# Kernel optimization log

Hardware: AMD Instinct MI355X
Metric: run time of the kernel (lower is better)

Reference implementation:

```python
import jax, jax.numpy as jnp
import numpy as np

N = 50000
E = 800000
F_IN, F_HID, F_OUT = 128, 128, 64


def setup_inputs() -> dict:
    key = jax.random.key(0)
    ks = jax.random.split(key, 8)
    x = jax.random.normal(ks[0], (N, F_IN), dtype=jnp.float32)
    attn_edge_index = jax.random.randint(ks[1], (2, E), 0, N, dtype=jnp.int64)
    attn_edge_weight = jax.random.uniform(ks[2], (E,), dtype=jnp.float32)
    # GCNConv params (glorot-ish scale); PyG lin has no bias, conv bias added after aggregation
    W1 = jax.random.normal(ks[3], (F_IN, F_HID), dtype=jnp.float32) * (1.0 / np.sqrt(F_IN))
    b1 = jnp.zeros((F_HID,), dtype=jnp.float32)
    W2 = jax.random.normal(ks[4], (F_HID, F_OUT), dtype=jnp.float32) * (1.0 / np.sqrt(F_HID))
    b2 = jnp.zeros((F_OUT,), dtype=jnp.float32)
    return {"x": x, "attn_edge_index": attn_edge_index, "attn_edge_weight": attn_edge_weight,
            "W1": W1, "b1": b1, "W2": W2, "b2": b2}


def _gcn_norm(edge_index, edge_weight, num_nodes):
    # Add self-loops with weight 1 (PyG gcn_norm default)
    loop = jnp.arange(num_nodes, dtype=edge_index.dtype)
    src = jnp.concatenate([edge_index[0], loop])
    dst = jnp.concatenate([edge_index[1], loop])
    w = jnp.concatenate([edge_weight, jnp.ones((num_nodes,), edge_weight.dtype)])
    deg = jax.ops.segment_sum(w, dst, num_segments=num_nodes)  # in-degree weighted
    dinv = jnp.where(deg > 0, jax.lax.rsqrt(deg), 0.0)
    norm = dinv[src] * w * dinv[dst]  # symmetric normalization
    return src, dst, norm


def _gcn_conv(h, src, dst, norm, W, b, num_nodes):
    h = h @ W                                   # [N, Fout] dense transform
    msg = norm[:, None] * h[src]                # [E+N, Fout] gather-multiply
    out = jax.ops.segment_sum(msg, dst, num_segments=num_nodes)  # scatter-add
    return out + b


def reference(x, attn_edge_index, attn_edge_weight, W1, b1, W2, b2):
    num_nodes = x.shape[0]
    src, dst, norm = _gcn_norm(attn_edge_index, attn_edge_weight, num_nodes)
    h = _gcn_conv(x, src, dst, norm, W1, b1, num_nodes)
    h = jax.nn.relu(h)
    # dropout(p=0.5) is identity in eval mode
    h = _gcn_conv(h, src, dst, norm, W2, b2, num_nodes)
    return h
```

## Files before the change

### kernel.cpp

```cpp
#include <hip/hip_runtime.h>
#include <hip/hip_bf16.h>

static constexpr int FIN   = 128;
static constexpr int FHID  = 128;
static constexpr int FOUTC = 64;
static constexpr int CAP   = 64;

typedef short bf16x8 __attribute__((ext_vector_type(8)));
typedef float f32x4 __attribute__((ext_vector_type(4)));
typedef unsigned u32x2 __attribute__((ext_vector_type(2)));
typedef unsigned u32x4 __attribute__((ext_vector_type(4)));

__device__ __forceinline__ float bfbits2f(unsigned short u) {
  union { unsigned i; float f; } c; c.i = ((unsigned)u) << 16; return c.f;
}
__device__ __forceinline__ float wbits2f(unsigned u) {
  union { unsigned i; float f; } c; c.i = u; return c.f;
}
__device__ __forceinline__ unsigned f2wbits(float f) {
  union { float fv; unsigned i; } c; c.fv = f; return c.i;
}
__device__ __forceinline__ void unpack_bf2(unsigned u, float& lo, float& hi) {
  union { unsigned i; float f; } a, b;
  a.i = u << 16;
  b.i = u & 0xffff0000u;
  lo = a.f; hi = b.f;
}
__device__ __forceinline__ unsigned short f2bfbits(float f) {
  union { float fv; unsigned i; } c; c.fv = f;
  unsigned i = c.i;
  unsigned r = i + 0x7FFFu + ((i >> 16) & 1u);
  if ((i & 0x7F800000u) == 0x7F800000u) r = i;
  return (unsigned short)(r >> 16);
}
__device__ __forceinline__ int ld_idx(const void* ei, int is64, long long off) {
  return is64 ? (int)((const long long*)ei)[off] : ((const int*)ei)[off];
}
__device__ __forceinline__ float ld_f(const void* p, int isbf, long long i) {
  return isbf ? bfbits2f(((const unsigned short*)p)[i]) : ((const float*)p)[i];
}

__global__ void setup_kernel(const unsigned short* __restrict__ xb,
                             const unsigned* __restrict__ eiw,
                             const void* __restrict__ W1, const void* __restrict__ W2,
                             int* __restrict__ flags, unsigned short* __restrict__ Wt1,
                             unsigned short* __restrict__ Wt2, uint4* __restrict__ ellz,
                             int nell4) {
  const int tid = threadIdx.x;
  const int gid = blockIdx.x * 256 + tid;
  __shared__ int sflags[2];
  if (tid < 64) {
    unsigned short xs = xb[2 * tid];
    unsigned long long mb = __ballot(((xs >> 7) & 0xFFu) >= 0xC0u);
    unsigned long long m2 = __ballot(eiw[2 * tid + 1] != 0u);
    if (tid == 0) {
      sflags[0] = (mb == 0ull);
      sflags[1] = (m2 == 0ull);
      if (blockIdx.x == 0) { flags[0] = sflags[0]; flags[1] = sflags[1]; }
    }
  }
  __syncthreads();
  int f = sflags[0];
  if (blockIdx.x < 96) {
    int i = gid;
    if (i < 128 * 128) {
      int k = i >> 7, nn = i & 127;
      Wt1[nn * 128 + k] = f2bfbits(ld_f(W1, f, i));
    } else {
      int j = i - 128 * 128;
      int k = j >> 6, nn = j & 63;
      Wt2[nn * 128 + k] = f2bfbits(ld_f(W2, f, j));
    }
  }
  uint4 z = make_uint4(0u, 0u, 0u, 0u);
  for (int j = gid; j < nell4; j += gridDim.x * 256) ellz[j] = z;
}

__global__ void fill_ell(const void* __restrict__ ei, const void* __restrict__ ew,
                         const int* __restrict__ flg, unsigned long long* __restrict__ ell,
                         int E, int half) {
  int g = blockIdx.x * 256 + threadIdx.x;
  if (g >= half) return;
  int is64 = flg[1], isbf = flg[0];
  int sA = ld_idx(ei, is64, g);
  int dA = ld_idx(ei, is64, (long long)E + g);
  unsigned wA = f2wbits(ld_f(ew, isbf, g));
  int eB = g + half;
  bool hasB = eB < E;
  int sB = 0, dB = 0;
  unsigned wB = 0u;
  if (hasB) {
    sB = ld_idx(ei, is64, eB);
    dB = ld_idx(ei, is64, (long long)E + eB);
    wB = f2wbits(ld_f(ew, isbf, eB));
  }
  unsigned long long vA = ((unsigned long long)wA << 32) | (unsigned)sA;
  unsigned long long vB = ((unsigned long long)wB << 32) | (unsigned)sB;
  unsigned long long* rowA = ell + (size_t)dA * CAP;
  unsigned long long* rowB = ell + (size_t)dB * CAP;
  int pA = g & (CAP - 1), pB = eB & (CAP - 1);
  bool doneA = (vA == 0ull);
  bool doneB = !hasB || (vB == 0ull);
  unsigned long long oA = doneA ? 0ull : atomicCAS(&rowA[pA], 0ull, vA);
  unsigned long long oB = doneB ? 0ull : atomicCAS(&rowB[pB], 0ull, vB);
  for (int t = 1; t < CAP && !doneA && oA != 0ull; ++t) {
    pA = (pA + 1) & (CAP - 1);
    oA = atomicCAS(&rowA[pA], 0ull, vA);
  }
  for (int t = 1; t < CAP && !doneB && oB != 0ull; ++t) {
    pB = (pB + 1) & (CAP - 1);
    oB = atomicCAS(&rowB[pB], 0ull, vB);
  }
}

__global__ void dinv_compact(uint2* __restrict__ ell, float* __restrict__ dinv,
                             unsigned* __restrict__ cedge, int n) {
  int wid = (blockIdx.x * 256 + threadIdx.x) >> 6;
  int lane = threadIdx.x & 63;
  if (wid >= n) return;
  u32x2 rv = __builtin_nontemporal_load((const u32x2*)(ell + (size_t)wid * CAP) + lane);
  float w = wbits2f(rv.y);
  float ws = w;
#pragma unroll
  for (int off = 1; off < 64; off <<= 1) ws += __shfl_xor(ws, off);
  bool valid = rv.y != 0u;
  unsigned long long m = __ballot(valid);
  int c = __popcll(m);
  int rank = __popcll(m & ((1ull << lane) - 1ull));
  int destl = valid ? rank : c + (lane - rank);
  unsigned entry = valid ? ((rv.x << 16) | (unsigned)f2bfbits(w)) : 0u;
  int pe = __builtin_amdgcn_ds_permute(destl << 2, (int)entry);
  cedge[(size_t)wid * (CAP * 2) + lane] = (unsigned)pe;
  if (lane == 0) dinv[wid] = rsqrtf(1.f + ws);
}

__launch_bounds__(256)
__global__ void gather_l1(const void* __restrict__ x, const int* __restrict__ flg,
                          const unsigned* __restrict__ cedge, const float* __restrict__ dinv,
                          unsigned* __restrict__ agg, int n) {
  int wid = (blockIdx.x * 256 + threadIdx.x) >> 6;
  int lane = threadIdx.x & 63;
  if (wid >= n) return;
  unsigned e = __builtin_nontemporal_load(cedge + (size_t)wid * (CAP * 2) + lane);
  unsigned long long m = __ballot(e != 0u);
  int c = __popcll(m);
  float di = dinv[wid];
  int rs = (lane < c) ? (int)(e >> 16) : wid;
  float dsrc = dinv[rs];
  float wv = (lane < c) ? bfbits2f((unsigned short)(e & 0xFFFFu)) : 1.f;
  int cp = c + 1; if (cp > 64) cp = 64;
  float rw = (lane < cp) ? wv * dsrc : 0.f;
  int iters = (cp + 15) >> 4;

  if (flg[0]) {
    const uint4* xv = (const uint4*)x;
    const int fgrp = lane & 15, egrp = lane >> 4;
    float acc[8];
#pragma unroll
    for (int k = 0; k < 8; ++k) acc[k] = 0.f;

#define L1_LOAD(UA, UB, UC, UD, WA, WB, WC, WD, base)                       \
    {                                                                       \
      int i0 = (base) + egrp, i1 = i0 + 4, i2 = i0 + 8, i3 = i0 + 12;       \
      int s0 = __shfl(rs, i0), s1 = __shfl(rs, i1);                         \
      int s2 = __shfl(rs, i2), s3 = __shfl(rs, i3);                         \
      UA = xv[(size_t)s0 * 16 + fgrp];                                      \
      UB = xv[(size_t)s1 * 16 + fgrp];                                      \
      UC = xv[(size_t)s2 * 16 + fgrp];                                      \
      UD = xv[(size_t)s3 * 16 + fgrp];                                      \
      WA = __shfl(rw, i0); WB = __shfl(rw, i1);                             \
      WC = __shfl(rw, i2); WD = __shfl(rw, i3);                             \
    }
#define L1_FMA(U, W)                                                        \
    { float l, h;                                                           \
      unpack_bf2(U.x, l, h); acc[0]=fmaf(W,l,acc[0]); acc[1]=fmaf(W,h,acc[1]); \
      unpack_bf2(U.y, l, h); acc[2]=fmaf(W,l,acc[2]); acc[3]=fmaf(W,h,acc[3]); \
      unpack_bf2(U.z, l, h); acc[4]=fmaf(W,l,acc[4]); acc[5]=fmaf(W,h,acc[5]); \
      unpack_bf2(U.w, l, h); acc[6]=fmaf(W,l,acc[6]); acc[7]=fmaf(W,h,acc[7]); }
#define L1_FMA4(UA,UB,UC,UD,WA,WB,WC,WD) \
    L1_FMA(UA,WA) L1_FMA(UB,WB) L1_FMA(UC,WC) L1_FMA(UD,WD)

    uint4 a0, a1, a2, a3, b0, b1, b2, b3;
    float wa0, wa1, wa2, wa3, wb0, wb1, wb2, wb3;
    L1_LOAD(a0, a1, a2, a3, wa0, wa1, wa2, wa3, 0);
    if (iters > 1) {
      L1_LOAD(b0, b1, b2, b3, wb0, wb1, wb2, wb3, 16);
      L1_FMA4(a0, a1, a2, a3, wa0, wa1, wa2, wa3);
      if (iters > 2) {
        L1_LOAD(a0, a1, a2, a3, wa0, wa1, wa2, wa3, 32);
        L1_FMA4(b0, b1, b2, b3, wb0, wb1, wb2, wb3);
        if (iters > 3) {
          L1_LOAD(b0, b1, b2, b3, wb0, wb1, wb2, wb3, 48);
          L1_FMA4(a0, a1, a2, a3, wa0, wa1, wa2, wa3);
          L1_FMA4(b0, b1, b2, b3, wb0, wb1, wb2, wb3);
        } else {
          L1_FMA4(a0, a1, a2, a3, wa0, wa1, wa2, wa3);
        }
      } else {
        L1_FMA4(b0, b1, b2, b3, wb0, wb1, wb2, wb3);
      }
    } else {
      L1_FMA4(a0, a1, a2, a3, wa0, wa1, wa2, wa3);
    }
#undef L1_LOAD
#undef L1_FMA
#undef L1_FMA4

#pragma unroll
    for (int k = 0; k < 8; ++k) {
      acc[k] += __shfl_xor(acc[k], 16);
      acc[k] += __shfl_xor(acc[k], 32);
    }
    if (lane < 16) {
      float o0 = di * acc[0], o1 = di * acc[1], o2 = di * acc[2], o3 = di * acc[3];
      float o4 = di * acc[4], o5 = di * acc[5], o6 = di * acc[6], o7 = di * acc[7];
      u32x4 pk;
      pk.x = (unsigned)f2bfbits(o0) | ((unsigned)f2bfbits(o1) << 16);
      pk.y = (unsigned)f2bfbits(o2) | ((unsigned)f2bfbits(o3) << 16);
      pk.z = (unsigned)f2bfbits(o4) | ((unsigned)f2bfbits(o5) << 16);
      pk.w = (unsigned)f2bfbits(o6) | ((unsigned)f2bfbits(o7) << 16);
      __builtin_nontemporal_store(pk, (u32x4*)agg + (size_t)wid * 16 + fgrp);
    }
  } else {
    const float4* xf = (const float4*)x;
    const int fgrp = lane & 31, egrp = lane >> 5;
    float acc[4] = {0.f, 0.f, 0.f, 0.f};
    int it8 = (cp + 7) >> 3;
    for (int it = 0; it < it8; ++it) {
      int b = it * 8 + egrp;
#pragma unroll
      for (int t = 0; t < 4; ++t) {
        int idx = b + t * 2;
        int s = __shfl(rs, idx);
        float w = __shfl(rw, idx);
        float4 v = xf[(size_t)s * 32 + fgrp];
        acc[0] = fmaf(w, v.x, acc[0]); acc[1] = fmaf(w, v.y, acc[1]);
        acc[2] = fmaf(w, v.z, acc[2]); acc[3] = fmaf(w, v.w, acc[3]);
      }
    }
#pragma unroll
    for (int k = 0; k < 4; ++k) acc[k] += __shfl_xor(acc[k], 32);
    if (lane < 32) {
      float o0 = di * acc[0], o1 = di * acc[1], o2 = di * acc[2], o3 = di * acc[3];
      uint2 pk;
      pk.x = (unsigned)f2bfbits(o0) | ((unsigned)f2bfbits(o1) << 16);
      pk.y = (unsigned)f2bfbits(o2) | ((unsigned)f2bfbits(o3) << 16);
      ((uint2*)agg)[(size_t)wid * 32 + fgrp] = pk;
    }
  }
}

__launch_bounds__(256)
__global__ void gather_l2(const unsigned short* __restrict__ hw2, const int* __restrict__ flg,
                          const unsigned* __restrict__ cedge, const float* __restrict__ dinv,
                          const void* __restrict__ b2, void* __restrict__ out, int n) {
  int wid = (blockIdx.x * 256 + threadIdx.x) >> 6;
  int lane = threadIdx.x & 63;
  if (wid >= n) return;
  unsigned e = __builtin_nontemporal_load(cedge + (size_t)wid * (CAP * 2) + lane);
  unsigned long long m = __ballot(e != 0u);
  int c = __popcll(m);
  float di = dinv[wid];
  int rs = (lane < c) ? (int)(e >> 16) : wid;
  float dsrc = dinv[rs];
  float wv = (lane < c) ? bfbits2f((unsigned short)(e & 0xFFFFu)) : 1.f;
  int cp = c + 1; if (cp > 64) cp = 64;
  float rw = (lane < cp) ? wv * dsrc : 0.f;
  int iters = (cp + 15) >> 4;

  const uint4* hv = (const uint4*)hw2;
  const int fgrp = lane & 7, egrp = lane >> 3;
  float acc[8];
#pragma unroll
  for (int k = 0; k < 8; ++k) acc[k] = 0.f;

#define L2_LOAD(UA, UB, WA, WB, base)                                   \
  { int i0 = (base) + egrp, i1 = i0 + 8;                                \
    int s0 = __shfl(rs, i0), s1 = __shfl(rs, i1);                       \
    UA = hv[(size_t)s0 * 8 + fgrp];                                     \
    UB = hv[(size_t)s1 * 8 + fgrp];                                     \
    WA = __shfl(rw, i0); WB = __shfl(rw, i1); }
#define L2_FMA(U, W)                                                    \
  { float l, h;                                                         \
    unpack_bf2(U.x, l, h); acc[0]=fmaf(W,l,acc[0]); acc[1]=fmaf(W,h,acc[1]); \
    unpack_bf2(U.y, l, h); acc[2]=fmaf(W,l,acc[2]); acc[3]=fmaf(W,h,acc[3]); \
    unpack_bf2(U.z, l, h); acc[4]=fmaf(W,l,acc[4]); acc[5]=fmaf(W,h,acc[5]); \
    unpack_bf2(U.w, l, h); acc[6]=fmaf(W,l,acc[6]); acc[7]=fmaf(W,h,acc[7]); }
#define L2_FMA2(UA, UB, WA, WB) L2_FMA(UA, WA) L2_FMA(UB, WB)

  uint4 a0, a1, b0, b1;
  float wa0, wa1, wb0, wb1;
  L2_LOAD(a0, a1, wa0, wa1, 0);
  if (iters > 1) {
    L2_LOAD(b0, b1, wb0, wb1, 16);
    L2_FMA2(a0, a1, wa0, wa1);
    if (iters > 2) {
      L2_LOAD(a0, a1, wa0, wa1, 32);
      L2_FMA2(b0, b1, wb0, wb1);
      if (iters > 3) {
        L2_LOAD(b0, b1, wb0, wb1, 48);
        L2_FMA2(a0, a1, wa0, wa1);
        L2_FMA2(b0, b1, wb0, wb1);
      } else {
        L2_FMA2(a0, a1, wa0, wa1);
      }
    } else {
      L2_FMA2(b0, b1, wb0, wb1);
    }
  } else {
    L2_FMA2(a0, a1, wa0, wa1);
  }
#undef L2_LOAD
#undef L2_FMA
#undef L2_FMA2

#pragma unroll
  for (int k = 0; k < 8; ++k) {
    acc[k] += __shfl_xor(acc[k], 8);
    acc[k] += __shfl_xor(acc[k], 16);
    acc[k] += __shfl_xor(acc[k], 32);
  }
  if (lane < 8) {
    int isbf = flg[0];
    float o0 = di * acc[0] + ld_f(b2, isbf, fgrp * 8 + 0);
    float o1 = di * acc[1] + ld_f(b2, isbf, fgrp * 8 + 1);
    float o2 = di * acc[2] + ld_f(b2, isbf, fgrp * 8 + 2);
    float o3 = di * acc[3] + ld_f(b2, isbf, fgrp * 8 + 3);
    float o4 = di * acc[4] + ld_f(b2, isbf, fgrp * 8 + 4);
    float o5 = di * acc[5] + ld_f(b2, isbf, fgrp * 8 + 5);
    float o6 = di * acc[6] + ld_f(b2, isbf, fgrp * 8 + 6);
    float o7 = di * acc[7] + ld_f(b2, isbf, fgrp * 8 + 7);
    if (isbf) {
      uint4 pk;
      pk.x = (unsigned)f2bfbits(o0) | ((unsigned)f2bfbits(o1) << 16);
      pk.y = (unsigned)f2bfbits(o2) | ((unsigned)f2bfbits(o3) << 16);
      pk.z = (unsigned)f2bfbits(o4) | ((unsigned)f2bfbits(o5) << 16);
      pk.w = (unsigned)f2bfbits(o6) | ((unsigned)f2bfbits(o7) << 16);
      ((uint4*)out)[(size_t)wid * 8 + fgrp] = pk;
    } else {
      ((float4*)out)[(size_t)wid * 16 + fgrp * 2 + 0] = make_float4(o0, o1, o2, o3);
      ((float4*)out)[(size_t)wid * 16 + fgrp * 2 + 1] = make_float4(o4, o5, o6, o7);
    }
  }
}

__launch_bounds__(256)
__global__ void gemm12(const unsigned short* __restrict__ agg1,
                       const unsigned short* __restrict__ Wt1,
                       const unsigned short* __restrict__ Wt2,
                       const void* __restrict__ b1, const int* __restrict__ flg,
                       unsigned short* __restrict__ hw2, int M) {
  __shared__ unsigned short As[128 * 128];
  __shared__ unsigned short W1s[128 * 128];
  __shared__ unsigned short W2s[64 * 128];
  const int tid = threadIdx.x;
  const int r0 = blockIdx.x * 128;

  for (int i = tid; i < 128 * 16; i += 256) {
    int r = i >> 4, ch = i & 15;
    uint4 v = make_uint4(0u, 0u, 0u, 0u);
    if (r0 + r < M) v = *(const uint4*)(agg1 + (size_t)(r0 + r) * 128 + ch * 8);
    *(uint4*)&As[r * 128 + ((ch ^ (r & 15)) << 3)] = v;
  }
  for (int i = tid; i < 128 * 16; i += 256) {
    int r = i >> 4, ch = i & 15;
    uint4 v = *(const uint4*)(Wt1 + (size_t)r * 128 + ch * 8);
    *(uint4*)&W1s[r * 128 + ((ch ^ (r & 15)) << 3)] = v;
  }
  for (int i = tid; i < 64 * 16; i += 256) {
    int r = i >> 4, ch = i & 15;
    uint4 v = *(const uint4*)(Wt2 + (size_t)r * 128 + ch * 8);
    *(uint4*)&W2s[r * 128 + ((ch ^ (r & 15)) << 3)] = v;
  }
  __syncthreads();

  const int lane = tid & 63;
  const int wv = tid >> 6;
  const int ln15 = lane & 15;
  const int kq = lane >> 4;
  const int wbf = flg[0];

  f32x4 acc1[2][8];
#pragma unroll
  for (int mi = 0; mi < 2; ++mi)
#pragma unroll
    for (int nt = 0; nt < 8; ++nt) acc1[mi][nt] = (f32x4){0.f, 0.f, 0.f, 0.f};
#pragma unroll
  for (int kc = 0; kc < 4; ++kc) {
    int coff = (((kc * 4 + kq) ^ ln15) << 3);
    bf16x8 a0 = *(const bf16x8*)&As[((2 * wv + 0) * 16 + ln15) * 128 + coff];
    bf16x8 a1 = *(const bf16x8*)&As[((2 * wv + 1) * 16 + ln15) * 128 + coff];
#pragma unroll
    for (int nt = 0; nt < 8; ++nt) {
      bf16x8 b = *(const bf16x8*)&W1s[(nt * 16 + ln15) * 128 + coff];
      acc1[0][nt] = __builtin_amdgcn_mfma_f32_16x16x32_bf16(a0, b, acc1[0][nt], 0, 0, 0);
      acc1[1][nt] = __builtin_amdgcn_mfma_f32_16x16x32_bf16(a1, b, acc1[1][nt], 0, 0, 0);
    }
  }

#pragma unroll
  for (int nt = 0; nt < 8; ++nt) {
    int col = nt * 16 + ln15;
    float bv = ld_f(b1, wbf, col);
#pragma unroll
    for (int mi = 0; mi < 2; ++mi) {
#pragma unroll
      for (int r = 0; r < 4; ++r) {
        int row = 32 * wv + mi * 16 + kq * 4 + r;
        float o = fmaxf(acc1[mi][nt][r] + bv, 0.f);
        As[row * 128 + ((((col >> 3)) ^ (row & 15)) << 3) + (col & 7)] = f2bfbits(o);
      }
    }
  }
  __syncthreads();

  f32x4 acc2[2][4];
#pragma unroll
  for (int mi = 0; mi < 2; ++mi)
#pragma unroll
    for (int nt = 0; nt < 4; ++nt) acc2[mi][nt] = (f32x4){0.f, 0.f, 0.f, 0.f};
#pragma unroll
  for (int kc = 0; kc < 4; ++kc) {
    int coff = (((kc * 4 + kq) ^ ln15) << 3);
    bf16x8 a0 = *(const bf16x8*)&As[((2 * wv + 0) * 16 + ln15) * 128 + coff];
    bf16x8 a1 = *(const bf16x8*)&As[((2 * wv + 1) * 16 + ln15) * 128 + coff];
#pragma unroll
    for (int nt = 0; nt < 4; ++nt) {
      bf16x8 b = *(const bf16x8*)&W2s[(nt * 16 + ln15) * 128 + coff];
      acc2[0][nt] = __builtin_amdgcn_mfma_f32_16x16x32_bf16(a0, b, acc2[0][nt], 0, 0, 0);
      acc2[1][nt] = __builtin_amdgcn_mfma_f32_16x16x32_bf16(a1, b, acc2[1][nt], 0, 0, 0);
    }
  }
#pragma unroll
  for (int nt = 0; nt < 4; ++nt) {
    int col = nt * 16 + ln15;
#pragma unroll
    for (int mi = 0; mi < 2; ++mi) {
#pragma unroll
      for (int r = 0; r < 4; ++r) {
        int gr = r0 + 32 * wv + mi * 16 + kq * 4 + r;
        if (gr < M) hw2[(size_t)gr * 64 + col] = f2bfbits(acc2[mi][nt][r]);
      }
    }
  }
}

extern "C" void kernel_launch(void* const* d_in, const int* in_sizes, int n_in, void* d_out,
                              int out_size, void* d_ws, size_t ws_size, hipStream_t stream) {
  const void* x  = d_in[0];
  const void* ei = d_in[1];
  const void* ew = d_in[2];
  const void* W1 = d_in[3];
  const void* b1 = d_in[4];
  const void* W2 = d_in[5];
  const void* b2 = d_in[6];

  const int N = in_sizes[0] / FIN;
  const int E = in_sizes[1] / 2;
  const int B = 256;

  int* flags   = (int*)d_ws;
  float* dinv  = (float*)(flags + 16);
  unsigned short* Wt1 = (unsigned short*)(dinv + N);
  unsigned short* Wt2 = Wt1 + 128 * 128;
  unsigned long long* ell = (unsigned long long*)(Wt2 + 64 * 128);
  unsigned* cedge = (unsigned*)ell;
  unsigned short* agg1 = (unsigned short*)(ell + (size_t)N * CAP);
  unsigned short* hw2  = agg1 + (size_t)N * FHID;

  const int half = (E + 1) / 2;
  setup_kernel<<<512, B, 0, stream>>>((const unsigned short*)x, (const unsigned*)ei, W1, W2,
                                      flags, Wt1, Wt2, (uint4*)ell, N * CAP / 2);
  fill_ell<<<(half + B - 1) / B, B, 0, stream>>>(ei, ew, flags, ell, E, half);
  dinv_compact<<<(N + 3) / 4, B, 0, stream>>>((uint2*)ell, dinv, cedge, N);
  gather_l1<<<(N + 3) / 4, B, 0, stream>>>(x, flags, cedge, dinv, (unsigned*)agg1, N);
  gemm12<<<(N + 127) / 128, B, 0, stream>>>(agg1, Wt1, Wt2, b1, flags, hw2, N);
  gather_l2<<<(N + 3) / 4, B, 0, stream>>>(hw2, flags, cedge, dinv, b2, d_out, N);
}
```

Baseline: 231.3 us.

## Pack ELL entries into 32 bits and accumulate degree with atomics

Changes the ELL adjacency from 64-bit (src, fp32 weight) entries to 32-bit entries packing the source index with a bf16 weight, and compacts the table in place. Weighted in-degree is accumulated via float atomicAdd during fill instead of a wave reduction over the table. This halves the memory zeroed, written by CAS and re-read by the compaction and gather kernels. In exchange it adds one atomic per edge on the degree array, and the degree's summation order becomes nondeterministic.

```diff
diff --git a/kernel.cpp b/kernel.cpp
--- a/kernel.cpp
+++ b/kernel.cpp
@@ -8,17 +8,10 @@
 
 typedef short bf16x8 __attribute__((ext_vector_type(8)));
 typedef float f32x4 __attribute__((ext_vector_type(4)));
-typedef unsigned u32x2 __attribute__((ext_vector_type(2)));
 typedef unsigned u32x4 __attribute__((ext_vector_type(4)));
 
 __device__ __forceinline__ float bfbits2f(unsigned short u) {
   union { unsigned i; float f; } c; c.i = ((unsigned)u) << 16; return c.f;
-}
-__device__ __forceinline__ float wbits2f(unsigned u) {
-  union { unsigned i; float f; } c; c.i = u; return c.f;
-}
-__device__ __forceinline__ unsigned f2wbits(float f) {
-  union { float fv; unsigned i; } c; c.fv = f; return c.i;
 }
 __device__ __forceinline__ void unpack_bf2(unsigned u, float& lo, float& hi) {
   union { unsigned i; float f; } a, b;
@@ -44,8 +37,8 @@
                              const unsigned* __restrict__ eiw,
                              const void* __restrict__ W1, const void* __restrict__ W2,
                              int* __restrict__ flags, unsigned short* __restrict__ Wt1,
-                             unsigned short* __restrict__ Wt2, uint4* __restrict__ ellz,
-                             int nell4) {
+                             unsigned short* __restrict__ Wt2, uint4* __restrict__ zr,
+                             int nz4, int nztot) {
   const int tid = threadIdx.x;
   const int gid = blockIdx.x * 256 + tid;
   __shared__ int sflags[2];
@@ -73,65 +66,65 @@
     }
   }
   uint4 z = make_uint4(0u, 0u, 0u, 0u);
-  for (int j = gid; j < nell4; j += gridDim.x * 256) ellz[j] = z;
+  for (int j = gid; j < nz4; j += gridDim.x * 256) zr[j] = z;
+  if (gid == 0) {
+    for (int j = nz4 * 4; j < nztot; ++j) ((unsigned*)zr)[j] = 0u;
+  }
 }
 
 __global__ void fill_ell(const void* __restrict__ ei, const void* __restrict__ ew,
-                         const int* __restrict__ flg, unsigned long long* __restrict__ ell,
-                         int E, int half) {
+                         const int* __restrict__ flg, unsigned* __restrict__ ell,
+                         float* __restrict__ deg, int E, int half) {
   int g = blockIdx.x * 256 + threadIdx.x;
   if (g >= half) return;
   int is64 = flg[1], isbf = flg[0];
   int sA = ld_idx(ei, is64, g);
   int dA = ld_idx(ei, is64, (long long)E + g);
-  unsigned wA = f2wbits(ld_f(ew, isbf, g));
+  float wA = ld_f(ew, isbf, g);
   int eB = g + half;
   bool hasB = eB < E;
   int sB = 0, dB = 0;
-  unsigned wB = 0u;
+  float wB = 0.f;
   if (hasB) {
     sB = ld_idx(ei, is64, eB);
     dB = ld_idx(ei, is64, (long long)E + eB);
-    wB = f2wbits(ld_f(ew, isbf, eB));
-  }
-  unsigned long long vA = ((unsigned long long)wA << 32) | (unsigned)sA;
-  unsigned long long vB = ((unsigned long long)wB << 32) | (unsigned)sB;
-  unsigned long long* rowA = ell + (size_t)dA * CAP;
-  unsigned long long* rowB = ell + (size_t)dB * CAP;
+    wB = ld_f(ew, isbf, eB);
+  }
+  unsigned vA = (((unsigned)sA) << 16) | (unsigned)f2bfbits(wA);
+  unsigned vB = (((unsigned)sB) << 16) | (unsigned)f2bfbits(wB);
+  unsigned* rowA = ell + (size_t)dA * CAP;
+  unsigned* rowB = ell + (size_t)dB * CAP;
   int pA = g & (CAP - 1), pB = eB & (CAP - 1);
-  bool doneA = (vA == 0ull);
-  bool doneB = !hasB || (vB == 0ull);
-  unsigned long long oA = doneA ? 0ull : atomicCAS(&rowA[pA], 0ull, vA);
-  unsigned long long oB = doneB ? 0ull : atomicCAS(&rowB[pB], 0ull, vB);
-  for (int t = 1; t < CAP && !doneA && oA != 0ull; ++t) {
+  bool doneA = (vA == 0u);
+  bool doneB = !hasB || (vB == 0u);
+  unsigned oA = doneA ? 0u : atomicCAS(&rowA[pA], 0u, vA);
+  unsigned oB = doneB ? 0u : atomicCAS(&rowB[pB], 0u, vB);
+  if (!doneA) atomicAdd(&deg[dA], wA);
+  if (!doneB) atomicAdd(&deg[dB], wB);
+  for (int t = 1; t < CAP && !doneA && oA != 0u; ++t) {
     pA = (pA + 1) & (CAP - 1);
-    oA = atomicCAS(&rowA[pA], 0ull, vA);
-  }
-  for (int t = 1; t < CAP && !doneB && oB != 0ull; ++t) {
+    oA = atomicCAS(&rowA[pA], 0u, vA);
+  }
+  for (int t = 1; t < CAP && !doneB && oB != 0u; ++t) {
     pB = (pB + 1) & (CAP - 1);
-    oB = atomicCAS(&rowB[pB], 0ull, vB);
-  }
-}
-
-__global__ void dinv_compact(uint2* __restrict__ ell, float* __restrict__ dinv,
-                             unsigned* __restrict__ cedge, int n) {
+    oB = atomicCAS(&rowB[pB], 0u, vB);
+  }
+}
+
+__global__ void dinv_compact(unsigned* __restrict__ ell, const float* __restrict__ deg,
+                             float* __restrict__ dinv, int n) {
   int wid = (blockIdx.x * 256 + threadIdx.x) >> 6;
   int lane = threadIdx.x & 63;
   if (wid >= n) return;
-  u32x2 rv = __builtin_nontemporal_load((const u32x2*)(ell + (size_t)wid * CAP) + lane);
-  float w = wbits2f(rv.y);
-  float ws = w;
-#pragma unroll
-  for (int off = 1; off < 64; off <<= 1) ws += __shfl_xor(ws, off);
-  bool valid = rv.y != 0u;
+  unsigned rv = __builtin_nontemporal_load(ell + (size_t)wid * CAP + lane);
+  bool valid = rv != 0u;
   unsigned long long m = __ballot(valid);
   int c = __popcll(m);
   int rank = __popcll(m & ((1ull << lane) - 1ull));
   int destl = valid ? rank : c + (lane - rank);
-  unsigned entry = valid ? ((rv.x << 16) | (unsigned)f2bfbits(w)) : 0u;
-  int pe = __builtin_amdgcn_ds_permute(destl << 2, (int)entry);
-  cedge[(size_t)wid * (CAP * 2) + lane] = (unsigned)pe;
-  if (lane == 0) dinv[wid] = rsqrtf(1.f + ws);
+  int pe = __builtin_amdgcn_ds_permute(destl << 2, (int)rv);
+  ell[(size_t)wid * CAP + lane] = (unsigned)pe;
+  if (lane == 0) dinv[wid] = rsqrtf(1.f + deg[wid]);
 }
 
 __launch_bounds__(256)
@@ -141,7 +134,7 @@
   int wid = (blockIdx.x * 256 + threadIdx.x) >> 6;
   int lane = threadIdx.x & 63;
   if (wid >= n) return;
-  unsigned e = __builtin_nontemporal_load(cedge + (size_t)wid * (CAP * 2) + lane);
+  unsigned e = __builtin_nontemporal_load(cedge + (size_t)wid * CAP + lane);
   unsigned long long m = __ballot(e != 0u);
   int c = __popcll(m);
   float di = dinv[wid];
@@ -257,7 +250,7 @@
   int wid = (blockIdx.x * 256 + threadIdx.x) >> 6;
   int lane = threadIdx.x & 63;
   if (wid >= n) return;
-  unsigned e = __builtin_nontemporal_load(cedge + (size_t)wid * (CAP * 2) + lane);
+  unsigned e = __builtin_nontemporal_load(cedge + (size_t)wid * CAP + lane);
   unsigned long long m = __ballot(e != 0u);
   int c = __popcll(m);
   float di = dinv[wid];
@@ -463,16 +456,19 @@
   float* dinv  = (float*)(flags + 16);
   unsigned short* Wt1 = (unsigned short*)(dinv + N);
   unsigned short* Wt2 = Wt1 + 128 * 128;
-  unsigned long long* ell = (unsigned long long*)(Wt2 + 64 * 128);
-  unsigned* cedge = (unsigned*)ell;
+  float* deg   = (float*)(Wt2 + 64 * 128);
+  unsigned* ell = (unsigned*)(deg + N);
+  unsigned* cedge = ell;
   unsigned short* agg1 = (unsigned short*)(ell + (size_t)N * CAP);
   unsigned short* hw2  = agg1 + (size_t)N * FHID;
 
   const int half = (E + 1) / 2;
+  const int nztot = N + N * CAP;
+  const int nz4 = nztot >> 2;
   setup_kernel<<<512, B, 0, stream>>>((const unsigned short*)x, (const unsigned*)ei, W1, W2,
-                                      flags, Wt1, Wt2, (uint4*)ell, N * CAP / 2);
-  fill_ell<<<(half + B - 1) / B, B, 0, stream>>>(ei, ew, flags, ell, E, half);
-  dinv_compact<<<(N + 3) / 4, B, 0, stream>>>((uint2*)ell, dinv, cedge, N);
+                                      flags, Wt1, Wt2, (uint4*)deg, nz4, nztot);
+  fill_ell<<<(half + B - 1) / B, B, 0, stream>>>(ei, ew, flags, ell, deg, E, half);
+  dinv_compact<<<(N + 3) / 4, B, 0, stream>>>(ell, deg, dinv, N);
   gather_l1<<<(N + 3) / 4, B, 0, stream>>>(x, flags, cedge, dinv, (unsigned*)agg1, N);
   gemm12<<<(N + 127) / 128, B, 0, stream>>>(agg1, Wt1, Wt2, b1, flags, hw2, N);
   gather_l2<<<(N + 3) / 4, B, 0, stream>>>(hw2, flags, cedge, dinv, b2, d_out, N);
```

After: 279.3 us. 20.8% more time.

## Split layer-2 features into two column halves and gather in two phases

Applied to the files above, without the earlier changes.

gemm12 now writes the layer-2 transformed features as two separate N×32 bf16 arrays instead of one N×64 array. gather_l2 processes the two halves in sequence, using 4 lanes per source row with 16 edges per load step. The aim is to shrink the per-phase gather footprint to 64-byte rows so the randomly gathered data has better cache locality. In exchange, the shuffle reductions, edge-index shuffles and bias/output code run twice. Since each wave runs both phases back to back, the whole grid still touches both halves at the same time, so the locality gain may be small.

```diff
diff --git a/kernel.cpp b/kernel.cpp
--- a/kernel.cpp
+++ b/kernel.cpp
@@ -251,7 +251,9 @@
 }
 
 __launch_bounds__(256)
-__global__ void gather_l2(const unsigned short* __restrict__ hw2, const int* __restrict__ flg,
+__global__ void gather_l2(const unsigned short* __restrict__ hw2a,
+                          const unsigned short* __restrict__ hw2b,
+                          const int* __restrict__ flg,
                           const unsigned* __restrict__ cedge, const float* __restrict__ dinv,
                           const void* __restrict__ b2, void* __restrict__ out, int n) {
   int wid = (blockIdx.x * 256 + threadIdx.x) >> 6;
@@ -267,81 +269,75 @@
   int cp = c + 1; if (cp > 64) cp = 64;
   float rw = (lane < cp) ? wv * dsrc : 0.f;
   int iters = (cp + 15) >> 4;
-
-  const uint4* hv = (const uint4*)hw2;
-  const int fgrp = lane & 7, egrp = lane >> 3;
-  float acc[8];
-#pragma unroll
-  for (int k = 0; k < 8; ++k) acc[k] = 0.f;
-
-#define L2_LOAD(UA, UB, WA, WB, base)                                   \
-  { int i0 = (base) + egrp, i1 = i0 + 8;                                \
-    int s0 = __shfl(rs, i0), s1 = __shfl(rs, i1);                       \
-    UA = hv[(size_t)s0 * 8 + fgrp];                                     \
-    UB = hv[(size_t)s1 * 8 + fgrp];                                     \
-    WA = __shfl(rw, i0); WB = __shfl(rw, i1); }
+  const int fgrp = lane & 3, egrp = lane >> 2;
+  const int isbf = flg[0];
+
 #define L2_FMA(U, W)                                                    \
   { float l, h;                                                         \
     unpack_bf2(U.x, l, h); acc[0]=fmaf(W,l,acc[0]); acc[1]=fmaf(W,h,acc[1]); \
     unpack_bf2(U.y, l, h); acc[2]=fmaf(W,l,acc[2]); acc[3]=fmaf(W,h,acc[3]); \
     unpack_bf2(U.z, l, h); acc[4]=fmaf(W,l,acc[4]); acc[5]=fmaf(W,h,acc[5]); \
     unpack_bf2(U.w, l, h); acc[6]=fmaf(W,l,acc[6]); acc[7]=fmaf(W,h,acc[7]); }
-#define L2_FMA2(UA, UB, WA, WB) L2_FMA(UA, WA) L2_FMA(UB, WB)
-
-  uint4 a0, a1, b0, b1;
-  float wa0, wa1, wb0, wb1;
-  L2_LOAD(a0, a1, wa0, wa1, 0);
-  if (iters > 1) {
-    L2_LOAD(b0, b1, wb0, wb1, 16);
-    L2_FMA2(a0, a1, wa0, wa1);
-    if (iters > 2) {
-      L2_LOAD(a0, a1, wa0, wa1, 32);
-      L2_FMA2(b0, b1, wb0, wb1);
-      if (iters > 3) {
-        L2_LOAD(b0, b1, wb0, wb1, 48);
-        L2_FMA2(a0, a1, wa0, wa1);
-        L2_FMA2(b0, b1, wb0, wb1);
-      } else {
-        L2_FMA2(a0, a1, wa0, wa1);
-      }
-    } else {
-      L2_FMA2(b0, b1, wb0, wb1);
-    }
-  } else {
-    L2_FMA2(a0, a1, wa0, wa1);
-  }
-#undef L2_LOAD
+#define L2_LOAD1(U, W, base)                                            \
+  { int i0 = (base) + egrp; int s0 = __shfl(rs, i0);                    \
+    U = hv[(size_t)s0 * 4 + fgrp]; W = __shfl(rw, i0); }
+#define L2_PHASE(HV, PH)                                                \
+  {                                                                     \
+    const uint4* hv = (const uint4*)(HV);                               \
+    float acc[8];                                                       \
+    _Pragma("unroll") for (int k = 0; k < 8; ++k) acc[k] = 0.f;         \
+    uint4 a0, b0; float wa0, wb0;                                       \
+    L2_LOAD1(a0, wa0, 0)                                                \
+    if (iters > 1) {                                                    \
+      L2_LOAD1(b0, wb0, 16)                                             \
+      L2_FMA(a0, wa0)                                                   \
+      if (iters > 2) {                                                  \
+        L2_LOAD1(a0, wa0, 32)                                           \
+        L2_FMA(b0, wb0)                                                 \
+        if (iters > 3) {                                                \
+          L2_LOAD1(b0, wb0, 48)                                         \
+          L2_FMA(a0, wa0)                                               \
+          L2_FMA(b0, wb0)                                               \
+        } else { L2_FMA(a0, wa0) }                                      \
+      } else { L2_FMA(b0, wb0) }                                        \
+    } else { L2_FMA(a0, wa0) }                                          \
+    _Pragma("unroll") for (int k = 0; k < 8; ++k) {                     \
+      acc[k] += __shfl_xor(acc[k], 4);                                  \
+      acc[k] += __shfl_xor(acc[k], 8);                                  \
+      acc[k] += __shfl_xor(acc[k], 16);                                 \
+      acc[k] += __shfl_xor(acc[k], 32);                                 \
+    }                                                                   \
+    if (lane < 4) {                                                     \
+      int cb = (PH) * 32 + fgrp * 8;                                    \
+      float o0 = di * acc[0] + ld_f(b2, isbf, cb + 0);                  \
+      float o1 = di * acc[1] + ld_f(b2, isbf, cb + 1);                  \
+      float o2 = di * acc[2] + ld_f(b2, isbf, cb + 2);                  \
+      float o3 = di * acc[3] + ld_f(b2, isbf, cb + 3);                  \
+      float o4 = di * acc[4] + ld_f(b2, isbf, cb + 4);                  \
+      float o5 = di * acc[5] + ld_f(b2, isbf, cb + 5);                  \
+      float o6 = di * acc[6] + ld_f(b2, isbf, cb + 6);                  \
+      float o7 = di * acc[7] + ld_f(b2, isbf, cb + 7);                  \
+      if (isbf) {                                                       \
+        uint4 pk;                                                       \
+        pk.x = (unsigned)f2bfbits(o0) | ((unsigned)f2bfbits(o1) << 16); \
+        pk.y = (unsigned)f2bfbits(o2) | ((unsigned)f2bfbits(o3) << 16); \
+        pk.z = (unsigned)f2bfbits(o4) | ((unsigned)f2bfbits(o5) << 16); \
+        pk.w = (unsigned)f2bfbits(o6) | ((unsigned)f2bfbits(o7) << 16); \
+        ((uint4*)out)[(size_t)wid * 8 + (PH) * 4 + fgrp] = pk;          \
+      } else {                                                          \
+        ((float4*)out)[(size_t)wid * 16 + (PH) * 8 + fgrp * 2 + 0] =    \
+            make_float4(o0, o1, o2, o3);                                \
+        ((float4*)out)[(size_t)wid * 16 + (PH) * 8 + fgrp * 2 + 1] =    \
+            make_float4(o4, o5, o6, o7);                                \
+      }                                                                 \
+    }                                                                   \
+  }
+
+  L2_PHASE(hw2a, 0)
+  L2_PHASE(hw2b, 1)
+#undef L2_PHASE
+#undef L2_LOAD1
 #undef L2_FMA
-#undef L2_FMA2
-
-#pragma unroll
-  for (int k = 0; k < 8; ++k) {
-    acc[k] += __shfl_xor(acc[k], 8);
-    acc[k] += __shfl_xor(acc[k], 16);
-    acc[k] += __shfl_xor(acc[k], 32);
-  }
-  if (lane < 8) {
-    int isbf = flg[0];
-    float o0 = di * acc[0] + ld_f(b2, isbf, fgrp * 8 + 0);
-    float o1 = di * acc[1] + ld_f(b2, isbf, fgrp * 8 + 1);
-    float o2 = di * acc[2] + ld_f(b2, isbf, fgrp * 8 + 2);
-    float o3 = di * acc[3] + ld_f(b2, isbf, fgrp * 8 + 3);
-    float o4 = di * acc[4] + ld_f(b2, isbf, fgrp * 8 + 4);
-    float o5 = di * acc[5] + ld_f(b2, isbf, fgrp * 8 + 5);
-    float o6 = di * acc[6] + ld_f(b2, isbf, fgrp * 8 + 6);
-    float o7 = di * acc[7] + ld_f(b2, isbf, fgrp * 8 + 7);
-    if (isbf) {
-      uint4 pk;
-      pk.x = (unsigned)f2bfbits(o0) | ((unsigned)f2bfbits(o1) << 16);
-      pk.y = (unsigned)f2bfbits(o2) | ((unsigned)f2bfbits(o3) << 16);
-      pk.z = (unsigned)f2bfbits(o4) | ((unsigned)f2bfbits(o5) << 16);
-      pk.w = (unsigned)f2bfbits(o6) | ((unsigned)f2bfbits(o7) << 16);
-      ((uint4*)out)[(size_t)wid * 8 + fgrp] = pk;
-    } else {
-      ((float4*)out)[(size_t)wid * 16 + fgrp * 2 + 0] = make_float4(o0, o1, o2, o3);
-      ((float4*)out)[(size_t)wid * 16 + fgrp * 2 + 1] = make_float4(o4, o5, o6, o7);
-    }
-  }
 }
 
 __launch_bounds__(256)
@@ -349,7 +345,8 @@
                        const unsigned short* __restrict__ Wt1,
                        const unsigned short* __restrict__ Wt2,
                        const void* __restrict__ b1, const int* __restrict__ flg,
-                       unsigned short* __restrict__ hw2, int M) {
+                       unsigned short* __restrict__ hw2a, unsigned short* __restrict__ hw2b,
+                       int M) {
   __shared__ unsigned short As[128 * 128];
   __shared__ unsigned short W1s[128 * 128];
   __shared__ unsigned short W2s[64 * 128];
@@ -439,7 +436,11 @@
 #pragma unroll
       for (int r = 0; r < 4; ++r) {
         int gr = r0 + 32 * wv + mi * 16 + kq * 4 + r;
-        if (gr < M) hw2[(size_t)gr * 64 + col] = f2bfbits(acc2[mi][nt][r]);
+        if (gr < M) {
+          unsigned short v = f2bfbits(acc2[mi][nt][r]);
+          if (nt < 2) hw2a[(size_t)gr * 32 + col] = v;
+          else        hw2b[(size_t)gr * 32 + (col - 32)] = v;
+        }
       }
     }
   }
@@ -466,7 +467,8 @@
   unsigned long long* ell = (unsigned long long*)(Wt2 + 64 * 128);
   unsigned* cedge = (unsigned*)ell;
   unsigned short* agg1 = (unsigned short*)(ell + (size_t)N * CAP);
-  unsigned short* hw2  = agg1 + (size_t)N * FHID;
+  unsigned short* hw2a = agg1 + (size_t)N * FHID;
+  unsigned short* hw2b = hw2a + (size_t)N * 32;
 
   const int half = (E + 1) / 2;
   setup_kernel<<<512, B, 0, stream>>>((const unsigned short*)x, (const unsigned*)ei, W1, W2,
@@ -474,6 +476,6 @@
   fill_ell<<<(half + B - 1) / B, B, 0, stream>>>(ei, ew, flags, ell, E, half);
   dinv_compact<<<(N + 3) / 4, B, 0, stream>>>((uint2*)ell, dinv, cedge, N);
   gather_l1<<<(N + 3) / 4, B, 0, stream>>>(x, flags, cedge, dinv, (unsigned*)agg1, N);
-  gemm12<<<(N + 127) / 128, B, 0, stream>>>(agg1, Wt1, Wt2, b1, flags, hw2, N);
-  gather_l2<<<(N + 3) / 4, B, 0, stream>>>(hw2, flags, cedge, dinv, b2, d_out, N);
-}
+  gemm12<<<(N + 127) / 128, B, 0, stream>>>(agg1, Wt1, Wt2, b1, flags, hw2a, hw2b, N);
+  gather_l2<<<(N + 3) / 4, B, 0, stream>>>(hw2a, hw2b, flags, cedge, dinv, b2, d_out, N);
+}
```

Result: slower. 246.0 us (+6.4%).
